# Kernel optimization log

Hardware: AMD Instinct MI355X
Metric: run time of the kernel (lower is better)

The kernel has to match this reference:

```python
import jax, jax.numpy as jnp
import numpy as np

THRESHOLD = 0.8
SECONDARY = 0.5
SECONDARY_WEIGHT = 0.5
N_PATCH = 196  # 14*14 patches of 2x2 pixels from a 28x28 image


def setup_inputs() -> dict:
    key = jax.random.key(0)
    k = jax.random.split(key, 5)
    B = 4096
    x = jax.random.uniform(k[0], (B, 1, 28, 28), dtype=jnp.float32)
    W1 = jax.random.normal(k[1], (4, 32), dtype=jnp.float32) * 0.5
    b1 = jnp.zeros((32,), jnp.float32)
    W2 = jax.random.normal(k[2], (32, 10), dtype=jnp.float32) * 0.2
    b2 = jnp.zeros((10,), jnp.float32)
    return {"x": x, "W1": W1, "b1": b1, "W2": W2, "b2": b2}


def _forward(x, W1, b1, W2, b2):
    B = x.shape[0]
    img = x[:, 0]  # (B, 28, 28)
    # extract 2x2 stride-2 patches -> (B, 196, 4), pixel order (0,0),(0,1),(1,0),(1,1)
    patches = img.reshape(B, 14, 2, 14, 2).transpose(0, 1, 3, 2, 4).reshape(B, N_PATCH, 4)
    # quantum patch encoder surrogate: PauliZ expectation after RY(theta) encoding is cos(theta)
    q = jnp.cos(patches)  # (B, 196, 4)
    # pairwise state fidelity = squared cosine similarity, via one batched matmul
    qn = q / (jnp.linalg.norm(q, axis=-1, keepdims=True) + 1e-12)
    fid = jnp.einsum('bnd,bmd->bnm', qn, qn) ** 2  # (B, 196, 196)
    # threshold-edge adjacency: 1.0 above threshold, secondary_weight in [secondary, threshold)
    adj = jnp.where(fid >= THRESHOLD, 1.0,
                    jnp.where(fid >= SECONDARY, SECONDARY_WEIGHT, 0.0))
    adj = jnp.where(jnp.eye(N_PATCH, dtype=bool), 0.0, adj)  # no self-edges (u<v pairs only)
    # GraphAggregation pools over all 196 nodes (all nodes are added to the graph)
    pooled = jnp.mean(q, axis=1)  # (B, 4)
    logits = (pooled @ W1 + b1) @ W2 + b2  # (B, 10)
    return logits, adj


def reference(x, W1, b1, W2, b2):
    return _forward(x, W1, b1, W2, b2)
```

## Files before the change

### kernel.cpp

```cpp
#include <hip/hip_runtime.h>
#include <math.h>


#define NP    196
#define NPIX  784
#define BLK   256
#define VPR   (NP / 4)
#define F4PI  (NP * NP / 4)
#define F4PP  (2 * F4PI)

typedef float f32x4 __attribute__((ext_vector_type(4)));

__global__ __launch_bounds__(BLK) void quanv_kernel(
    const float* __restrict__ x,
    const float* __restrict__ W1, const float* __restrict__ b1,
    const float* __restrict__ W2, const float* __restrict__ b2,
    float* __restrict__ logits, float* __restrict__ adj)
{
    __shared__ float q4[2][NP][4];
    __shared__ __align__(16) float qnT[2][4][NP];
    __shared__ float pooled[2][4];

    const int g   = blockIdx.x;
    const int tid = threadIdx.x;
    const int w   = tid >> 6;
    const int l   = tid & 63;
    const float* imgs = x + (size_t)g * (2 * NPIX);

    for (int p = tid; p < 2 * NPIX; p += BLK) {
        int im = (p >= NPIX);
        int pp = p - im * NPIX;
        int r = pp / 28;
        int c = pp - r * 28;
        int n  = (r >> 1) * 14 + (c >> 1);
        int dd = ((r & 1) << 1) | (c & 1);
        q4[im][n][dd] = cosf(imgs[p]);
    }
    __syncthreads();

    for (int t = tid; t < 2 * NP; t += BLK) {
        int im = (t >= NP);
        int n  = t - im * NP;
        float a0 = q4[im][n][0], a1 = q4[im][n][1];
        float a2 = q4[im][n][2], a3 = q4[im][n][3];
        float inv = 1.0f / (sqrtf(a0*a0 + a1*a1 + a2*a2 + a3*a3) + 1e-12f);
        qnT[im][0][n] = a0 * inv;
        qnT[im][1][n] = a1 * inv;
        qnT[im][2][n] = a2 * inv;
        qnT[im][3][n] = a3 * inv;
    }

    if (w < 2) {
        float s0 = 0.f, s1 = 0.f, s2 = 0.f, s3 = 0.f;
        for (int n = l; n < NP; n += 64) {
            s0 += q4[w][n][0]; s1 += q4[w][n][1];
            s2 += q4[w][n][2]; s3 += q4[w][n][3];
        }
        #pragma unroll
        for (int off = 32; off >= 1; off >>= 1) {
            s0 += __shfl_down(s0, off);
            s1 += __shfl_down(s1, off);
            s2 += __shfl_down(s2, off);
            s3 += __shfl_down(s3, off);
        }
        if (l == 0) {
            pooled[w][0] = s0 * (1.0f / NP);
            pooled[w][1] = s1 * (1.0f / NP);
            pooled[w][2] = s2 * (1.0f / NP);
            pooled[w][3] = s3 * (1.0f / NP);
        }
    }
    __syncthreads();

    if (tid < 20) {
        int im = (tid >= 10);
        int j  = tid - im * 10;
        float p0 = pooled[im][0], p1 = pooled[im][1];
        float p2 = pooled[im][2], p3 = pooled[im][3];
        float acc = b2[j];
        #pragma unroll
        for (int k = 0; k < 32; ++k) {
            float h = b1[k] + p0 * W1[0*32 + k] + p1 * W1[1*32 + k]
                            + p2 * W1[2*32 + k] + p3 * W1[3*32 + k];
            acc += h * W2[k*10 + j];
        }
        logits[(size_t)(2*g + im) * 10 + j] = acc;
    }

    f32x4* outp = reinterpret_cast<f32x4*>(adj) + (size_t)g * F4PP;
    for (int e4 = tid; e4 < F4PP; e4 += BLK) {
        int im  = (e4 >= F4PI);
        int rem = e4 - im * F4PI;
        int n   = rem / VPR;
        int m0  = (rem - n * VPR) * 4;

        float c0 = qnT[im][0][n], c1 = qnT[im][1][n];
        float c2 = qnT[im][2][n], c3 = qnT[im][3][n];
        f32x4 v0 = *reinterpret_cast<const f32x4*>(&qnT[im][0][m0]);
        f32x4 v1 = *reinterpret_cast<const f32x4*>(&qnT[im][1][m0]);
        f32x4 v2 = *reinterpret_cast<const f32x4*>(&qnT[im][2][m0]);
        f32x4 v3 = *reinterpret_cast<const f32x4*>(&qnT[im][3][m0]);

        f32x4 d = c0*v0 + c1*v1 + c2*v2 + c3*v3;
        f32x4 f = d * d;

        f32x4 o;
        o.x = (f.x >= 0.8f) ? 1.0f : ((f.x >= 0.5f) ? 0.5f : 0.0f);
        o.y = (f.y >= 0.8f) ? 1.0f : ((f.y >= 0.5f) ? 0.5f : 0.0f);
        o.z = (f.z >= 0.8f) ? 1.0f : ((f.z >= 0.5f) ? 0.5f : 0.0f);
        o.w = (f.w >= 0.8f) ? 1.0f : ((f.w >= 0.5f) ? 0.5f : 0.0f);

        o.x = (m0 + 0 == n) ? 0.0f : o.x;
        o.y = (m0 + 1 == n) ? 0.0f : o.y;
        o.z = (m0 + 2 == n) ? 0.0f : o.z;
        o.w = (m0 + 3 == n) ? 0.0f : o.w;

        __builtin_nontemporal_store(o, &outp[e4]);
    }
}

extern "C" void kernel_launch(void* const* d_in, const int* in_sizes, int n_in,
                              void* d_out, int out_size, void* d_ws, size_t ws_size,
                              hipStream_t stream) {
    const float* x  = (const float*)d_in[0];
    const float* W1 = (const float*)d_in[1];
    const float* b1 = (const float*)d_in[2];
    const float* W2 = (const float*)d_in[3];
    const float* b2 = (const float*)d_in[4];

    const int B = in_sizes[0] / NPIX;
    float* logits = (float*)d_out;
    float* adj    = logits + (size_t)B * 10;

    quanv_kernel<<<B / 2, BLK, 0, stream>>>(x, W1, b1, W2, b2, logits, adj);
}
```

Measured before the change: 137.4 us.

## Split into normalization prepass and grid-stride adjacency streaming kernel

Splits the fused kernel in two. A prepass handles eight images per block: it computes the cosines, the pooled logits and the normalized patch vectors, and writes them to workspace in both row and transposed layouts. A persistent grid-stride kernel with 1024 blocks then streams the adjacency output, reading those vectors from global memory and using plain stores instead of nontemporal ones. This aims to decouple the write-bound adjacency stream from the per-image setup and improve write throughput, at the cost of an extra launch, a workspace round trip and global loads in the hot loop.

```diff
diff --git a/kernel.cpp b/kernel.cpp
--- a/kernel.cpp
+++ b/kernel.cpp
@@ -7,28 +7,29 @@
 #define BLK   256
 #define VPR   (NP / 4)
 #define F4PI  (NP * NP / 4)
-#define F4PP  (2 * F4PI)
+#define IMGB  8
 
 typedef float f32x4 __attribute__((ext_vector_type(4)));
 
-__global__ __launch_bounds__(BLK) void quanv_kernel(
+__global__ __launch_bounds__(BLK) void qn_prepass(
     const float* __restrict__ x,
     const float* __restrict__ W1, const float* __restrict__ b1,
     const float* __restrict__ W2, const float* __restrict__ b2,
-    float* __restrict__ logits, float* __restrict__ adj)
+    float* __restrict__ logits,
+    float* __restrict__ qnA_g,
+    float* __restrict__ qnT_g)
 {
-    __shared__ float q4[2][NP][4];
-    __shared__ __align__(16) float qnT[2][4][NP];
-    __shared__ float pooled[2][4];
+    __shared__ float q4[IMGB][NP][4];
+    __shared__ float pooled[IMGB][4];
 
-    const int g   = blockIdx.x;
+    const int blk = blockIdx.x;
     const int tid = threadIdx.x;
     const int w   = tid >> 6;
     const int l   = tid & 63;
-    const float* imgs = x + (size_t)g * (2 * NPIX);
+    const float* imgs = x + (size_t)blk * (IMGB * NPIX);
 
-    for (int p = tid; p < 2 * NPIX; p += BLK) {
-        int im = (p >= NPIX);
+    for (int p = tid; p < IMGB * NPIX; p += BLK) {
+        int im = p / NPIX;
         int pp = p - im * NPIX;
         int r = pp / 28;
         int c = pp - r * 28;
@@ -38,23 +39,12 @@
     }
     __syncthreads();
 
-    for (int t = tid; t < 2 * NP; t += BLK) {
-        int im = (t >= NP);
-        int n  = t - im * NP;
-        float a0 = q4[im][n][0], a1 = q4[im][n][1];
-        float a2 = q4[im][n][2], a3 = q4[im][n][3];
-        float inv = 1.0f / (sqrtf(a0*a0 + a1*a1 + a2*a2 + a3*a3) + 1e-12f);
-        qnT[im][0][n] = a0 * inv;
-        qnT[im][1][n] = a1 * inv;
-        qnT[im][2][n] = a2 * inv;
-        qnT[im][3][n] = a3 * inv;
-    }
-
-    if (w < 2) {
+    for (int imw = 0; imw < 2; ++imw) {
+        int im = 2 * w + imw;
         float s0 = 0.f, s1 = 0.f, s2 = 0.f, s3 = 0.f;
         for (int n = l; n < NP; n += 64) {
-            s0 += q4[w][n][0]; s1 += q4[w][n][1];
-            s2 += q4[w][n][2]; s3 += q4[w][n][3];
+            s0 += q4[im][n][0]; s1 += q4[im][n][1];
+            s2 += q4[im][n][2]; s3 += q4[im][n][3];
         }
         #pragma unroll
         for (int off = 32; off >= 1; off >>= 1) {
@@ -64,16 +54,32 @@
             s3 += __shfl_down(s3, off);
         }
         if (l == 0) {
-            pooled[w][0] = s0 * (1.0f / NP);
-            pooled[w][1] = s1 * (1.0f / NP);
-            pooled[w][2] = s2 * (1.0f / NP);
-            pooled[w][3] = s3 * (1.0f / NP);
+            pooled[im][0] = s0 * (1.0f / NP);
+            pooled[im][1] = s1 * (1.0f / NP);
+            pooled[im][2] = s2 * (1.0f / NP);
+            pooled[im][3] = s3 * (1.0f / NP);
         }
+    }
+
+    for (int t = tid; t < IMGB * NP; t += BLK) {
+        int im = t / NP;
+        int n  = t - im * NP;
+        size_t gi = (size_t)(blk * IMGB + im);
+        float a0 = q4[im][n][0], a1 = q4[im][n][1];
+        float a2 = q4[im][n][2], a3 = q4[im][n][3];
+        float inv = 1.0f / (sqrtf(a0*a0 + a1*a1 + a2*a2 + a3*a3) + 1e-12f);
+        f32x4 v; v.x = a0*inv; v.y = a1*inv; v.z = a2*inv; v.w = a3*inv;
+        *reinterpret_cast<f32x4*>(qnA_g + (gi * NP + n) * 4) = v;
+        float* qt = qnT_g + gi * (4 * NP);
+        qt[0*NP + n] = v.x;
+        qt[1*NP + n] = v.y;
+        qt[2*NP + n] = v.z;
+        qt[3*NP + n] = v.w;
     }
     __syncthreads();
 
-    if (tid < 20) {
-        int im = (tid >= 10);
+    if (tid < IMGB * 10) {
+        int im = tid / 10;
         int j  = tid - im * 10;
         float p0 = pooled[im][0], p1 = pooled[im][1];
         float p2 = pooled[im][2], p3 = pooled[im][3];
@@ -84,24 +90,35 @@
                             + p2 * W1[2*32 + k] + p3 * W1[3*32 + k];
             acc += h * W2[k*10 + j];
         }
-        logits[(size_t)(2*g + im) * 10 + j] = acc;
+        logits[(size_t)(blk * IMGB + im) * 10 + j] = acc;
     }
+}
 
-    f32x4* outp = reinterpret_cast<f32x4*>(adj) + (size_t)g * F4PP;
-    for (int e4 = tid; e4 < F4PP; e4 += BLK) {
-        int im  = (e4 >= F4PI);
-        int rem = e4 - im * F4PI;
-        int n   = rem / VPR;
-        int m0  = (rem - n * VPR) * 4;
+__global__ __launch_bounds__(BLK) void adj_stream(
+    const float* __restrict__ qnA_g,
+    const float* __restrict__ qnT_g,
+    float* __restrict__ adj,
+    unsigned int totalF4)
+{
+    f32x4* out = reinterpret_cast<f32x4*>(adj);
+    const unsigned int stride = gridDim.x * BLK;
 
-        float c0 = qnT[im][0][n], c1 = qnT[im][1][n];
-        float c2 = qnT[im][2][n], c3 = qnT[im][3][n];
-        f32x4 v0 = *reinterpret_cast<const f32x4*>(&qnT[im][0][m0]);
-        f32x4 v1 = *reinterpret_cast<const f32x4*>(&qnT[im][1][m0]);
-        f32x4 v2 = *reinterpret_cast<const f32x4*>(&qnT[im][2][m0]);
-        f32x4 v3 = *reinterpret_cast<const f32x4*>(&qnT[im][3][m0]);
+    for (unsigned int e4 = blockIdx.x * BLK + threadIdx.x; e4 < totalF4;
+         e4 += stride) {
+        unsigned int b   = e4 / F4PI;
+        unsigned int rem = e4 - b * F4PI;
+        unsigned int n   = rem / VPR;
+        unsigned int m0  = (rem - n * VPR) * 4;
 
-        f32x4 d = c0*v0 + c1*v1 + c2*v2 + c3*v3;
+        const f32x4 c = *reinterpret_cast<const f32x4*>(
+            qnA_g + ((size_t)b * NP + n) * 4);
+        const float* qt = qnT_g + (size_t)b * (4 * NP);
+        f32x4 v0 = *reinterpret_cast<const f32x4*>(qt + 0*NP + m0);
+        f32x4 v1 = *reinterpret_cast<const f32x4*>(qt + 1*NP + m0);
+        f32x4 v2 = *reinterpret_cast<const f32x4*>(qt + 2*NP + m0);
+        f32x4 v3 = *reinterpret_cast<const f32x4*>(qt + 3*NP + m0);
+
+        f32x4 d = c.x*v0 + c.y*v1 + c.z*v2 + c.w*v3;
         f32x4 f = d * d;
 
         f32x4 o;
@@ -115,7 +132,7 @@
         o.z = (m0 + 2 == n) ? 0.0f : o.z;
         o.w = (m0 + 3 == n) ? 0.0f : o.w;
 
-        __builtin_nontemporal_store(o, &outp[e4]);
+        out[e4] = o;
     }
 }
 
@@ -132,5 +149,12 @@
     float* logits = (float*)d_out;
     float* adj    = logits + (size_t)B * 10;
 
-    quanv_kernel<<<B / 2, BLK, 0, stream>>>(x, W1, b1, W2, b2, logits, adj);
+    float* qnA_g = (float*)d_ws;
+    float* qnT_g = qnA_g + (size_t)B * NP * 4;
+
+    qn_prepass<<<B / IMGB, BLK, 0, stream>>>(x, W1, b1, W2, b2,
+                                             logits, qnA_g, qnT_g);
+
+    const unsigned int totalF4 = (unsigned int)B * F4PI;
+    adj_stream<<<1024, BLK, 0, stream>>>(qnA_g, qnT_g, adj, totalF4);
 }
```

Measured after the change: 218.1 us. 1.59x slower.
